# Performance work log

Measured on AMD Instinct MI355X. Metric: run time of the kernel, lower is better.

The kernel has to match this reference:

```python
import jax, jax.numpy as jnp
import numpy as np

L, H, D, V, TMAX = 6, 16, 1024, 32000, 2048
HD = D // H
EPS = 1e-5


def _ln(x, g, b):
    m = jnp.mean(x, axis=-1, keepdims=True)
    v = jnp.var(x, axis=-1, keepdims=True)
    return (x - m) * jax.lax.rsqrt(v + EPS) * g + b


def setup_inputs() -> dict:
    key = jax.random.key(0)
    ks = jax.random.split(key, 16)
    s = 0.02
    inp = {
        'idx': jax.random.randint(ks[0], (2, TMAX), 0, V),
        'targets': jax.random.randint(ks[1], (2, TMAX), 0, V),
        'tok_emb': jax.random.normal(ks[2], (V, D), jnp.float32) * s,
        'pos_emb': jax.random.normal(ks[3], (TMAX, D), jnp.float32) * s,
        'wq': jax.random.normal(ks[4], (L, D, D), jnp.float32) * s,
        'wk': jax.random.normal(ks[5], (L, D, D), jnp.float32) * s,
        'wv': jax.random.normal(ks[6], (L, D, D), jnp.float32) * s,
        'w_proj': jax.random.normal(ks[7], (L, D, D), jnp.float32) * s,
        'b_proj': jnp.zeros((L, D), jnp.float32),
        'w_fc1': jax.random.normal(ks[8], (L, D, 4 * D), jnp.float32) * s,
        'b_fc1': jnp.zeros((L, 4 * D), jnp.float32),
        'w_fc2': jax.random.normal(ks[9], (L, 4 * D, D), jnp.float32) * s,
        'b_fc2': jnp.zeros((L, D), jnp.float32),
        'ln1_g': jnp.ones((L, D), jnp.float32), 'ln1_b': jnp.zeros((L, D), jnp.float32),
        'ln2_g': jnp.ones((L, D), jnp.float32), 'ln2_b': jnp.zeros((L, D), jnp.float32),
        'lnf_g': jnp.ones((D,), jnp.float32), 'lnf_b': jnp.zeros((D,), jnp.float32),
        'w_head': jax.random.normal(ks[10], (D, V), jnp.float32) * s,
        'b_head': jnp.zeros((V,), jnp.float32),
    }
    return inp


def reference(idx, targets, tok_emb, pos_emb, wq, wk, wv, w_proj, b_proj,
              w_fc1, b_fc1, w_fc2, b_fc2, ln1_g, ln1_b, ln2_g, ln2_b,
              lnf_g, lnf_b, w_head, b_head):
    B, T = idx.shape
    x = tok_emb[idx] + pos_emb[:T]  # [B,T,D]
    causal = jnp.tril(jnp.ones((T, T), bool))
    scale = HD ** -0.5
    for l in range(L):
        h = _ln(x, ln1_g[l], ln1_b[l])
        q = (h @ wq[l]).reshape(B, T, H, HD)
        k = (h @ wk[l]).reshape(B, T, H, HD)
        v = (h @ wv[l]).reshape(B, T, H, HD)
        att = jnp.einsum('bqhd,bkhd->bhqk', q, k) * scale
        att = jnp.where(causal, att, -jnp.inf)
        att = jax.nn.softmax(att, axis=-1)  # dropout is identity in eval
        o = jnp.einsum('bhqk,bkhd->bqhd', att, v).reshape(B, T, D)
        x = x + o @ w_proj[l] + b_proj[l]
        h = _ln(x, ln2_g[l], ln2_b[l])
        x = x + jax.nn.relu(h @ w_fc1[l] + b_fc1[l]) @ w_fc2[l] + b_fc2[l]
    x = _ln(x, lnf_g, lnf_b)
    logits = x @ w_head + b_head  # [B,T,V]
    logp = jax.nn.log_softmax(logits, axis=-1)
    nll = -jnp.take_along_axis(logp, targets[..., None], axis=-1)[..., 0]
    loss = jnp.mean(nll)
    return logits, loss
```

## Files before the change

kernel.cpp:

```cpp
#include <hip/hip_runtime.h>

#define LAYERS 6
#define NH 16
#define DIM 1024
#define VOCAB 32000
#define SEQ 2048
#define NBATCH 2
#define HEADD 64
#define NROW (NBATCH*SEQ)
#define FF 4096
#define QKVS 3072
#define NCB (VOCAB/256)
#define LN_EPS 1e-5f

typedef unsigned short bfu;
typedef __attribute__((ext_vector_type(8))) short s16x8;
typedef __attribute__((ext_vector_type(4))) float f32x4;

__device__ __forceinline__ float bf2f(bfu u) { return __uint_as_float(((unsigned)u) << 16); }
__device__ __forceinline__ bfu f2bf(float x) {
  unsigned u = __float_as_uint(x);
  return (bfu)((u + 0x7fffu + ((u >> 16) & 1u)) >> 16);
}

__device__ __forceinline__ void gload16(const void* g, void* l) {
  __builtin_amdgcn_global_load_lds((const __attribute__((address_space(1))) void*)g,
                                   (__attribute__((address_space(3))) void*)l, 16, 0, 0);
}

__device__ __forceinline__ f32x4 mfma32(s16x8 a, s16x8 b, f32x4 c) {
  return __builtin_amdgcn_mfma_f32_16x16x32_bf16(a, b, c, 0, 0, 0);
}

__global__ __launch_bounds__(256) void tkernel(const float* __restrict__ in,
                                               bfu* __restrict__ out, int R, int C) {
  __shared__ bfu tile[32][33];
  int tx = threadIdx.x, ty = threadIdx.y;
  int bx = blockIdx.x * 32, by = blockIdx.y * 32;
#pragma unroll
  for (int i = 0; i < 4; ++i)
    tile[ty + i * 8][tx] = f2bf(in[(size_t)(by + ty + i * 8) * C + bx + tx]);
  __syncthreads();
#pragma unroll
  for (int i = 0; i < 4; ++i)
    out[(size_t)(bx + ty + i * 8) * R + by + tx] = tile[tx][ty + i * 8];
}

__global__ __launch_bounds__(256) void wtrans_kernel(const float* __restrict__ wq,
                                                     const float* __restrict__ wk,
                                                     const float* __restrict__ wv,
                                                     const float* __restrict__ wp,
                                                     const float* __restrict__ w1,
                                                     const float* __restrict__ w2,
                                                     bfu* __restrict__ qkvT,
                                                     bfu* __restrict__ wpT,
                                                     bfu* __restrict__ f1T,
                                                     bfu* __restrict__ f2T) {
  __shared__ bfu tile[32][33];
  int bi = blockIdx.x;
  const float* in; bfu* out; int R, C, id;
  if (bi < 4096) {
    int p = bi >> 10; id = bi & 1023;
    in = p == 0 ? wq : p == 1 ? wk : p == 2 ? wv : wp;
    out = (p == 3) ? wpT : qkvT + (size_t)p * DIM * DIM;
    R = DIM; C = DIM;
  } else if (bi < 8192) {
    id = bi - 4096; in = w1; out = f1T; R = DIM; C = FF;
  } else {
    id = bi - 8192; in = w2; out = f2T; R = FF; C = DIM;
  }
  int nbx = C >> 5;
  int bx = (id % nbx) * 32, by = (id / nbx) * 32;
  int tx = threadIdx.x, ty = threadIdx.y;
#pragma unroll
  for (int i = 0; i < 4; ++i)
    tile[ty + i * 8][tx] = f2bf(in[(size_t)(by + ty + i * 8) * C + bx + tx]);
  __syncthreads();
#pragma unroll
  for (int i = 0; i < 4; ++i)
    out[(size_t)(bx + ty + i * 8) * R + by + tx] = tile[tx][ty + i * 8];
}

__global__ __launch_bounds__(256) void vtrans_kernel(const bfu* __restrict__ qkvb,
                                                     bfu* __restrict__ vT) {
  __shared__ bfu tile[32][33];
  int bh = blockIdx.z;
  int b = bh >> 4, h = bh & 15;
  int t0 = blockIdx.x * 32, d0 = blockIdx.y * 32;
  int tx = threadIdx.x, ty = threadIdx.y;
  const bfu* in = qkvb + (size_t)b * SEQ * QKVS + 2048 + h * HEADD;
#pragma unroll
  for (int i = 0; i < 4; ++i)
    tile[ty + i * 8][tx] = in[(size_t)(t0 + ty + i * 8) * QKVS + d0 + tx];
  __syncthreads();
  bfu* out = vT + ((size_t)bh * HEADD) * SEQ;
#pragma unroll
  for (int i = 0; i < 4; ++i)
    out[(size_t)(d0 + ty + i * 8) * SEQ + t0 + tx] = tile[tx][ty + i * 8];
}

__global__ __launch_bounds__(256) void embed_kernel(const int* __restrict__ idx,
                                                    const float* __restrict__ tok,
                                                    const float* __restrict__ pos,
                                                    float* __restrict__ xf) {
  int row = blockIdx.x;
  int t = row % SEQ;
  int tokid = idx[row];
  int d0 = threadIdx.x * 4;
  float4 tv = *(const float4*)&tok[(size_t)tokid * DIM + d0];
  float4 pv = *(const float4*)&pos[(size_t)t * DIM + d0];
  float4 r;
  r.x = tv.x + pv.x; r.y = tv.y + pv.y; r.z = tv.z + pv.z; r.w = tv.w + pv.w;
  *(float4*)&xf[(size_t)row * DIM + d0] = r;
}

__global__ __launch_bounds__(256) void ln_kernel(const float* __restrict__ xf,
                                                 const float* __restrict__ gw,
                                                 const float* __restrict__ bw,
                                                 bfu* __restrict__ h) {
  const int row = blockIdx.x * 4 + (threadIdx.x >> 6);
  const int lane = threadIdx.x & 63;
  const float* xr = xf + (size_t)row * DIM;
  float4 xv[4];
  float s = 0.0f, ss = 0.0f;
#pragma unroll
  for (int j = 0; j < 4; ++j) {
    xv[j] = *(const float4*)&xr[lane * 4 + j * 256];
    s  += xv[j].x + xv[j].y + xv[j].z + xv[j].w;
    ss += xv[j].x * xv[j].x + xv[j].y * xv[j].y + xv[j].z * xv[j].z + xv[j].w * xv[j].w;
  }
#pragma unroll
  for (int o = 32; o; o >>= 1) { s += __shfl_xor(s, o); ss += __shfl_xor(ss, o); }
  float mean = s * (1.0f / DIM);
  float inv = rsqrtf(ss * (1.0f / DIM) - mean * mean + LN_EPS);
#pragma unroll
  for (int j = 0; j < 4; ++j) {
    float4 gv = *(const float4*)&gw[lane * 4 + j * 256];
    float4 bv = *(const float4*)&bw[lane * 4 + j * 256];
    ushort4 hv;
    hv.x = f2bf((xv[j].x - mean) * inv * gv.x + bv.x);
    hv.y = f2bf((xv[j].y - mean) * inv * gv.y + bv.y);
    hv.z = f2bf((xv[j].z - mean) * inv * gv.z + bv.z);
    hv.w = f2bf((xv[j].w - mean) * inv * gv.w + bv.w);
    *(ushort4*)&h[(size_t)row * DIM + lane * 4 + j * 256] = hv;
  }
}

template <int MODE>
__global__ __launch_bounds__(256) void gemm_bt(const bfu* __restrict__ A,
                                               const bfu* __restrict__ Bt,
                                               const float* __restrict__ bias,
                                               const float* resid,
                                               void* outp,
                                               int M, int N, int K) {
  __shared__ __align__(16) char sm[32768];
  const int tid = threadIdx.x;
  const int lane = tid & 63, wave = tid >> 6;
  const int c = lane & 15, g = lane >> 4;

  const int gx = gridDim.x, gy = gridDim.y;
  int orig = blockIdx.y * gx + blockIdx.x;
  int cpx = (gx * gy) >> 3;
  int swz = (orig & 7) * cpx + (orig >> 3);
  int by = swz / gx, bx = swz - by * gx;

  const int m0 = by * 128, n0 = bx * 128;
  const int wm = (wave & 1) * 64, wn = (wave >> 1) * 64;
  f32x4 acc[4][4] = {};
  const char* Ac = (const char*)A;
  const char* Bc = (const char*)Bt;
  const size_t stride = (size_t)K * 2;

  const int g1 = tid, g2 = tid + 256;
  const int r1 = g1 >> 2, j1 = g1 & 3;
  const int r2 = g2 >> 2, j2 = g2 & 3;
  const size_t a1 = (size_t)(m0 + r1) * stride + j1 * 16;
  const size_t a2 = (size_t)(m0 + r2) * stride + j2 * 16;
  const size_t b1 = (size_t)(n0 + r1) * stride + j1 * 16;
  const size_t b2 = (size_t)(n0 + r2) * stride + j2 * 16;

  auto STAGE = [&](int kt, int buf) {
    char* base = sm + buf * 16384;
    size_t ko = (size_t)kt * 64;
    gload16(Ac + a1 + ko, base + g1 * 16);
    gload16(Ac + a2 + ko, base + g2 * 16);
    gload16(Bc + b1 + ko, base + 8192 + g1 * 16);
    gload16(Bc + b2 + ko, base + 8192 + g2 * 16);
  };

  const int NT = K >> 5;
  STAGE(0, 0);
  STAGE(1, 1);
  asm volatile("s_waitcnt vmcnt(4)" ::: "memory");
  __builtin_amdgcn_s_barrier();
  __builtin_amdgcn_sched_barrier(0);

  for (int i = 0; i < NT; ++i) {
    const char* base = sm + (i & 1) * 16384;
    s16x8 af[4], bfr[4];
#pragma unroll
    for (int mi = 0; mi < 4; ++mi)
      af[mi] = *(const s16x8*)(base + (wm + mi * 16 + c) * 64 + g * 16);
#pragma unroll
    for (int ni = 0; ni < 4; ++ni)
      bfr[ni] = *(const s16x8*)(base + 8192 + (wn + ni * 16 + c) * 64 + g * 16);
    asm volatile("s_waitcnt lgkmcnt(0)" ::: "memory");
    __builtin_amdgcn_sched_barrier(0);
    __builtin_amdgcn_s_barrier();
    __builtin_amdgcn_sched_barrier(0);
    if (i + 2 < NT) STAGE(i + 2, i & 1);
    __builtin_amdgcn_s_setprio(1);
#pragma unroll
    for (int mi = 0; mi < 4; ++mi)
#pragma unroll
      for (int ni = 0; ni < 4; ++ni)
        acc[mi][ni] = mfma32(af[mi], bfr[ni], acc[mi][ni]);
    __builtin_amdgcn_s_setprio(0);
    if (i < NT - 2) {
      asm volatile("s_waitcnt vmcnt(4)" ::: "memory");
      __builtin_amdgcn_s_barrier();
      __builtin_amdgcn_sched_barrier(0);
    } else if (i == NT - 2) {
      asm volatile("s_waitcnt vmcnt(0)" ::: "memory");
      __builtin_amdgcn_s_barrier();
      __builtin_amdgcn_sched_barrier(0);
    }
  }

#pragma unroll
  for (int mi = 0; mi < 4; ++mi) {
#pragma unroll
    for (int ni = 0; ni < 4; ++ni) {
      int col = n0 + wn + ni * 16 + c;
      float bv = bias ? bias[col] : 0.0f;
#pragma unroll
      for (int jj = 0; jj < 4; ++jj) {
        int row = m0 + wm + mi * 16 + g * 4 + jj;
        float val = acc[mi][ni][jj] + bv;
        size_t oi = (size_t)row * N + col;
        if (MODE == 1) val = fmaxf(val, 0.0f);
        if (MODE == 2)      ((float*)outp)[oi] = resid[oi] + val;
        else if (MODE == 3) ((float*)outp)[oi] = val;
        else                ((bfu*)outp)[oi] = f2bf(val);
      }
    }
  }
}

template <int MODE>
__global__ __launch_bounds__(1024) void gemm1024(const bfu* __restrict__ A,
                                                 const bfu* __restrict__ Bt,
                                                 const float* __restrict__ bias,
                                                 const float* resid,
                                                 void* outp,
                                                 int M, int N, int K,
                                                 int colchunk,
                                                 float* __restrict__ pmax,
                                                 float* __restrict__ psum) {
  extern __shared__ char smem[];
  const int tid = threadIdx.x;
  const int lane = tid & 63, w = tid >> 6;
  const int c = lane & 15, g = lane >> 4;

  const int gx = gridDim.x, gy = gridDim.y;
  int orig = blockIdx.y * gx + blockIdx.x;
  int cpx = (gx * gy) >> 3;
  int swz = (orig & 7) * cpx + (orig >> 3);
  int bx, by;
  if (colchunk) { bx = swz / gy; by = swz - bx * gy; }
  else          { by = swz / gx; bx = swz - by * gx; }
  const int m0 = by * 256, n0 = bx * 256;

  const int wrow = w >> 2, wcol = w & 3;
  const size_t gstr = (size_t)K * 2;
  const char* Ag = (const char*)A + (size_t)m0 * gstr;
  const char* Bg = (const char*)Bt + (size_t)n0 * gstr;

  int srow0 = tid >> 3, scg0 = (tid & 7) ^ (srow0 & 7);
  int srow1 = (tid + 1024) >> 3, scg1 = (tid & 7) ^ (srow1 & 7);
  const size_t ga0 = (size_t)srow0 * gstr + scg0 * 16;
  const size_t ga1 = (size_t)srow1 * gstr + scg1 * 16;

  auto STAGE = [&](int kt, int buf) {
    char* base = smem + buf * 65536;
    size_t ko = (size_t)kt * 128;
    gload16(Ag + ga0 + ko, base + w * 1024);
    gload16(Ag + ga1 + ko, base + 16384 + w * 1024);
    gload16(Bg + ga0 + ko, base + 32768 + w * 1024);
    gload16(Bg + ga1 + ko, base + 49152 + w * 1024);
  };

  const int NT = K >> 6;
  f32x4 acc[4][4] = {};

  STAGE(0, 0);
  STAGE(1, 1);
  asm volatile("s_waitcnt vmcnt(4)" ::: "memory");
  __builtin_amdgcn_s_barrier();
  __builtin_amdgcn_sched_barrier(0);

  const int rsw = (c & 7) << 4;
  const int off0 = (g * 16) ^ rsw;
  const int off1 = (64 + g * 16) ^ rsw;

  for (int i = 0; i < NT; ++i) {
    const char* ldsA = smem + (i & 1) * 65536 + (wrow * 64 + c) * 128;
    const char* ldsB = smem + (i & 1) * 65536 + 32768 + (wcol * 64 + c) * 128;
    s16x8 a[4], b[4];
#pragma unroll
    for (int mi = 0; mi < 4; ++mi) a[mi] = *(const s16x8*)(ldsA + mi * 2048 + off0);
#pragma unroll
    for (int ni = 0; ni < 4; ++ni) b[ni] = *(const s16x8*)(ldsB + ni * 2048 + off0);
    __builtin_amdgcn_s_setprio(1);
#pragma unroll
    for (int mi = 0; mi < 4; ++mi)
#pragma unroll
      for (int ni = 0; ni < 4; ++ni)
        acc[mi][ni] = mfma32(a[mi], b[ni], acc[mi][ni]);
    __builtin_amdgcn_s_setprio(0);
#pragma unroll
    for (int mi = 0; mi < 4; ++mi) a[mi] = *(const s16x8*)(ldsA + mi * 2048 + off1);
#pragma unroll
    for (int ni = 0; ni < 4; ++ni) b[ni] = *(const s16x8*)(ldsB + ni * 2048 + off1);
    asm volatile("s_waitcnt lgkmcnt(0)" ::: "memory");
    __builtin_amdgcn_sched_barrier(0);
    __builtin_amdgcn_s_barrier();
    __builtin_amdgcn_sched_barrier(0);
    if (i + 2 < NT) STAGE(i + 2, i & 1);
    __builtin_amdgcn_s_setprio(1);
#pragma unroll
    for (int mi = 0; mi < 4; ++mi)
#pragma unroll
      for (int ni = 0; ni < 4; ++ni)
        acc[mi][ni] = mfma32(a[mi], b[ni], acc[mi][ni]);
    __builtin_amdgcn_s_setprio(0);
    if (i < NT - 2) {
      asm volatile("s_waitcnt vmcnt(4)" ::: "memory");
      __builtin_amdgcn_s_barrier();
      __builtin_amdgcn_sched_barrier(0);
    } else if (i == NT - 2) {
      asm volatile("s_waitcnt vmcnt(0)" ::: "memory");
      __builtin_amdgcn_s_barrier();
      __builtin_amdgcn_sched_barrier(0);
    }
  }

  if (MODE != 4) {
#pragma unroll
    for (int mi = 0; mi < 4; ++mi) {
#pragma unroll
      for (int ni = 0; ni < 4; ++ni) {
        int col = n0 + wcol * 64 + ni * 16 + c;
        float bv = bias ? bias[col] : 0.0f;
#pragma unroll
        for (int jj = 0; jj < 4; ++jj) {
          int row = m0 + wrow * 64 + mi * 16 + g * 4 + jj;
          float val = acc[mi][ni][jj] + bv;
          size_t oi = (size_t)row * N + col;
          if (MODE == 1) val = fmaxf(val, 0.0f);
          else if (MODE == 2) { ((float*)outp)[oi] = resid[oi] + val; continue; }
          if (MODE == 3) ((float*)outp)[oi] = val;
          else           ((bfu*)outp)[oi] = f2bf(val);
        }
      }
    }
  } else {
    float* sred = (float*)(smem + 131072);
    const int ncb = N >> 8;
    float bvv[4]; int colv[4];
#pragma unroll
    for (int ni = 0; ni < 4; ++ni) {
      colv[ni] = n0 + wcol * 64 + ni * 16 + c;
      bvv[ni] = bias ? bias[colv[ni]] : 0.0f;
    }
#pragma unroll
    for (int mi = 0; mi < 4; ++mi) {
#pragma unroll
      for (int jj = 0; jj < 4; ++jj) {
        int row = m0 + wrow * 64 + mi * 16 + g * 4 + jj;
        float v[4];
#pragma unroll
        for (int ni = 0; ni < 4; ++ni) {
          v[ni] = acc[mi][ni][jj] + bvv[ni];
          ((float*)outp)[(size_t)row * N + colv[ni]] = v[ni];
        }
        float mx = fmaxf(fmaxf(v[0], v[1]), fmaxf(v[2], v[3]));
#pragma unroll
        for (int off = 1; off < 16; off <<= 1) mx = fmaxf(mx, __shfl_xor(mx, off));
        float sm = __expf(v[0] - mx) + __expf(v[1] - mx) +
                   __expf(v[2] - mx) + __expf(v[3] - mx);
#pragma unroll
        for (int off = 1; off < 16; off <<= 1) sm += __shfl_xor(sm, off);
        if (c == 0) {
          int r64 = mi * 16 + g * 4 + jj;
          sred[(w * 64 + r64) * 2 + 0] = mx;
          sred[(w * 64 + r64) * 2 + 1] = sm;
        }
      }
    }
    __syncthreads();
    if (tid < 256) {
      int wr = tid >> 6, r64 = tid & 63;
      float M2 = -3.0e38f, S2 = 0.0f;
#pragma unroll
      for (int wc2 = 0; wc2 < 4; ++wc2) {
        float m_i = sred[((wr * 4 + wc2) * 64 + r64) * 2 + 0];
        float s_i = sred[((wr * 4 + wc2) * 64 + r64) * 2 + 1];
        float nm = fmaxf(M2, m_i);
        S2 = S2 * __expf(M2 - nm) + s_i * __expf(m_i - nm);
        M2 = nm;
      }
      size_t pi = (size_t)(m0 + tid) * ncb + bx;
      pmax[pi] = M2;
      psum[pi] = S2;
    }
  }
}

__global__ __launch_bounds__(512) void attn_kernel(const bfu* __restrict__ qkv,
                                                   const bfu* __restrict__ vT,
                                                   bfu* __restrict__ o) {
  __shared__ __align__(16) bfu Ks[64 * 64];
  __shared__ __align__(16) bfu Vt[64 * 64];
  __shared__ __align__(16) bfu Plds[8 * 16 * 32];
  const int tid = threadIdx.x;
  const int lane = tid & 63, w = tid >> 6;
  const int c = lane & 15, g = lane >> 4;
  const int qt = blockIdx.x, hh = blockIdx.y, b = blockIdx.z;
  const int q0 = qt * 128 + w * 16;
  const float SENT = -1e30f;
  const size_t rowb = (size_t)b * SEQ;

  const size_t qbase = (rowb + q0 + c) * QKVS + hh * HEADD + g * 8;
  s16x8 qf0 = *(const s16x8*)&qkv[qbase];
  s16x8 qf1 = *(const s16x8*)&qkv[qbase + 32];
  const bfu* Kg = qkv + 1024 + hh * HEADD;
  const bfu* vTb = vT + (size_t)(b * NH + hh) * HEADD * SEQ;
  bfu* Pw = Plds + w * 512;

  const int srow = tid >> 3;
  const int sgr = (tid & 7) ^ (srow & 7);
  const int cw = c & 7;

  f32x4 oacc[4] = {};
  float mrun = SENT, lrun = 0.0f;

  const int nkt = 2 * qt + 2;
  for (int kt = 0; kt < nkt; ++kt) {
    const int k0 = kt * 64;
    __syncthreads();
    gload16(Kg + (rowb + k0 + srow) * QKVS + sgr * 8, (char*)Ks + w * 1024);
    gload16(vTb + (size_t)srow * SEQ + k0 + sgr * 8, (char*)Vt + w * 1024);
    asm volatile("s_waitcnt vmcnt(0)" ::: "memory");
    __syncthreads();

#pragma unroll
    for (int s = 0; s < 2; ++s) {
      const int k0s = k0 + s * 32;
      if (k0s <= q0 + 15) {
        const char* Kb = (const char*)Ks + (size_t)(s * 32 + c) * 128;
        s16x8 kf00 = *(const s16x8*)(Kb + ((g ^ cw) * 16));
        s16x8 kf01 = *(const s16x8*)(Kb + (((4 + g) ^ cw) * 16));
        s16x8 kf10 = *(const s16x8*)(Kb + 16 * 128 + ((g ^ cw) * 16));
        s16x8 kf11 = *(const s16x8*)(Kb + 16 * 128 + (((4 + g) ^ cw) * 16));
        f32x4 s0 = {}, s1 = {};
        s0 = mfma32(kf00, qf0, s0); s0 = mfma32(kf01, qf1, s0);
        s1 = mfma32(kf10, qf0, s1); s1 = mfma32(kf11, qf1, s1);

        float sv[8];
#pragma unroll
        for (int jj = 0; jj < 4; ++jj) {
          int ka = k0s + g * 4 + jj, kb = ka + 16;
          sv[jj]     = (ka <= q0 + c) ? s0[jj] * 0.125f : SENT;
          sv[4 + jj] = (kb <= q0 + c) ? s1[jj] * 0.125f : SENT;
        }
        float tmax = sv[0];
#pragma unroll
        for (int i = 1; i < 8; ++i) tmax = fmaxf(tmax, sv[i]);
        tmax = fmaxf(tmax, __shfl_xor(tmax, 16));
        tmax = fmaxf(tmax, __shfl_xor(tmax, 32));

        bool defer = __all(tmax <= mrun + 8.0f) && (kt | s);
        float mref = defer ? mrun : fmaxf(mrun, tmax);
        float p[8], psm = 0.0f;
#pragma unroll
        for (int i = 0; i < 8; ++i) { p[i] = __expf(sv[i] - mref); psm += p[i]; }
        psm += __shfl_xor(psm, 16);
        psm += __shfl_xor(psm, 32);

        ushort4 w0; w0.x = f2bf(p[0]); w0.y = f2bf(p[1]); w0.z = f2bf(p[2]); w0.w = f2bf(p[3]);
        ushort4 w1; w1.x = f2bf(p[4]); w1.y = f2bf(p[5]); w1.z = f2bf(p[6]); w1.w = f2bf(p[7]);
        *(ushort4*)&Pw[c * 32 + g * 4] = w0;
        *(ushort4*)&Pw[c * 32 + 16 + g * 4] = w1;
        asm volatile("s_waitcnt lgkmcnt(0)" ::: "memory");
        __builtin_amdgcn_sched_barrier(0);

        if (defer) {
          lrun += psm;
        } else {
          float mnew = mref;
          float alpha = __expf(mrun - mnew);
          lrun = lrun * alpha + psm;
          mrun = mnew;
          float aq[4];
#pragma unroll
          for (int jj = 0; jj < 4; ++jj) aq[jj] = __shfl(alpha, g * 4 + jj);
#pragma unroll
          for (int dg = 0; dg < 4; ++dg)
#pragma unroll
            for (int jj = 0; jj < 4; ++jj) oacc[dg][jj] *= aq[jj];
        }

        ushort4 ra = *(const ushort4*)&Pw[c * 32 + g * 8];
        ushort4 rb = *(const ushort4*)&Pw[c * 32 + g * 8 + 4];
        s16x8 pa = {(short)ra.x, (short)ra.y, (short)ra.z, (short)ra.w,
                    (short)rb.x, (short)rb.y, (short)rb.z, (short)rb.w};

#pragma unroll
        for (int dg = 0; dg < 4; ++dg) {
          s16x8 vf = *(const s16x8*)((const char*)Vt + (size_t)(dg * 16 + c) * 128 +
                                     (((s * 4 + g) ^ cw) * 16));
          oacc[dg] = mfma32(pa, vf, oacc[dg]);
        }
      }
    }
  }

  float lq[4];
#pragma unroll
  for (int jj = 0; jj < 4; ++jj) lq[jj] = __shfl(lrun, g * 4 + jj);
#pragma unroll
  for (int dg = 0; dg < 4; ++dg)
#pragma unroll
    for (int jj = 0; jj < 4; ++jj) {
      size_t oi = (size_t)(rowb + q0 + g * 4 + jj) * DIM + hh * HEADD + dg * 16 + c;
      o[oi] = f2bf(oacc[dg][jj] / lq[jj]);
    }
}

__global__ __launch_bounds__(64) void nll_finish(const float* __restrict__ pmax,
                                                 const float* __restrict__ psum,
                                                 const float* __restrict__ logits,
                                                 const int* __restrict__ tgt,
                                                 float* __restrict__ nll) {
  int row = blockIdx.x, lane = threadIdx.x;
  const float* pm = pmax + (size_t)row * NCB;
  const float* ps = psum + (size_t)row * NCB;
  float m = -3.0e38f, s = 0.0f;
  if (lane < NCB) { m = pm[lane]; s = ps[lane]; }
  int i2 = lane + 64;
  if (i2 < NCB) {
    float m2 = pm[i2], s2 = ps[i2];
    float nm = fmaxf(m, m2);
    s = s * __expf(m - nm) + s2 * __expf(m2 - nm);
    m = nm;
  }
#pragma unroll
  for (int off = 32; off; off >>= 1) {
    float om = __shfl_xor(m, off), os = __shfl_xor(s, off);
    float nm = fmaxf(m, om);
    s = s * __expf(m - nm) + os * __expf(om - nm);
    m = nm;
  }
  if (lane == 0)
    nll[row] = (m + __logf(s)) - logits[(size_t)row * VOCAB + tgt[row]];
}

__global__ __launch_bounds__(256) void loss_kernel(const float* __restrict__ nll,
                                                   float* __restrict__ out) {
  float s = 0.0f;
  for (int i = threadIdx.x; i < NROW; i += 256) s += nll[i];
  for (int off = 32; off; off >>= 1) s += __shfl_xor(s, off);
  __shared__ float r[4];
  int wave = threadIdx.x >> 6;
  if ((threadIdx.x & 63) == 0) r[wave] = s;
  __syncthreads();
  if (threadIdx.x == 0) out[(size_t)NROW * VOCAB] = (r[0] + r[1] + r[2] + r[3]) * (1.0f / NROW);
}

extern "C" void kernel_launch(void* const* d_in, const int* in_sizes, int n_in,
                              void* d_out, int out_size, void* d_ws, size_t ws_size,
                              hipStream_t stream) {
  (void)in_sizes; (void)n_in; (void)out_size;
  const int* idx       = (const int*)d_in[0];
  const int* targets   = (const int*)d_in[1];
  const float* tok_emb = (const float*)d_in[2];
  const float* pos_emb = (const float*)d_in[3];
  const float* wq      = (const float*)d_in[4];
  const float* wk      = (const float*)d_in[5];
  const float* wv      = (const float*)d_in[6];
  const float* w_proj  = (const float*)d_in[7];
  const float* b_proj  = (const float*)d_in[8];
  const float* w_fc1   = (const float*)d_in[9];
  const float* b_fc1   = (const float*)d_in[10];
  const float* w_fc2   = (const float*)d_in[11];
  const float* b_fc2   = (const float*)d_in[12];
  const float* ln1_g   = (const float*)d_in[13];
  const float* ln1_b   = (const float*)d_in[14];
  const float* ln2_g   = (const float*)d_in[15];
  const float* ln2_b   = (const float*)d_in[16];
  const float* lnf_g   = (const float*)d_in[17];
  const float* lnf_b   = (const float*)d_in[18];
  const float* w_head  = (const float*)d_in[19];
  const float* b_head  = (const float*)d_in[20];

  char* ws = (char*)d_ws;
  size_t off = 0;
  auto alloc = [&](size_t bytes) {
    char* p = ws + off;
    off += (bytes + 255) & ~(size_t)255;
    return p;
  };
  float* xf   = (float*)alloc((size_t)NROW * DIM * 4);
  bfu* hbuf   = (bfu*)alloc((size_t)NROW * DIM * 2);
  bfu* qkvb   = (bfu*)alloc((size_t)NROW * QKVS * 2);
  bfu* ob     = (bfu*)alloc((size_t)NROW * DIM * 2);
  bfu* ub     = (bfu*)alloc((size_t)NROW * FF * 2);
  bfu* vT     = (bfu*)alloc((size_t)NROW * DIM * 2);
  bfu* qkvT   = (bfu*)alloc((size_t)QKVS * DIM * 2);
  bfu* wpT    = (bfu*)alloc((size_t)DIM * DIM * 2);
  bfu* f1T    = (bfu*)alloc((size_t)DIM * FF * 2);
  bfu* f2T    = (bfu*)alloc((size_t)DIM * FF * 2);
  bfu* hT     = (bfu*)alloc((size_t)DIM * VOCAB * 2);
  float* nll  = (float*)alloc((size_t)NROW * 4);
  float* pmax = (float*)alloc((size_t)NROW * NCB * 4);
  float* psum = (float*)alloc((size_t)NROW * NCB * 4);
  if (off > ws_size) return;

  const size_t LDSB = 131072;
  dim3 tb(32, 8);
  tkernel<<<dim3(VOCAB / 32, DIM / 32), tb, 0, stream>>>(w_head, hT, DIM, VOCAB);
  embed_kernel<<<NROW, 256, 0, stream>>>(idx, tok_emb, pos_emb, xf);

  float* logits = (float*)d_out;
  for (int l = 0; l < LAYERS; ++l) {
    const size_t wo = (size_t)l * DIM * DIM, fo = (size_t)l * DIM * FF;
    wtrans_kernel<<<12288, tb, 0, stream>>>(wq + wo, wk + wo, wv + wo, w_proj + wo,
                                            w_fc1 + fo, w_fc2 + fo, qkvT, wpT, f1T, f2T);
    ln_kernel<<<NROW / 4, 256, 0, stream>>>(xf, ln1_g + l * DIM, ln1_b + l * DIM, hbuf);
    gemm_bt<0><<<dim3(QKVS / 128, NROW / 128), 256, 0, stream>>>(
        hbuf, qkvT, nullptr, nullptr, qkvb, NROW, QKVS, DIM);
    vtrans_kernel<<<dim3(SEQ / 32, HEADD / 32, NBATCH * NH), tb, 0, stream>>>(qkvb, vT);
    attn_kernel<<<dim3(SEQ / 128, NH, NBATCH), 512, 0, stream>>>(qkvb, vT, ob);
    gemm_bt<2><<<dim3(DIM / 128, NROW / 128), 256, 0, stream>>>(
        ob, wpT, b_proj + l * DIM, xf, xf, NROW, DIM, DIM);
    ln_kernel<<<NROW / 4, 256, 0, stream>>>(xf, ln2_g + l * DIM, ln2_b + l * DIM, hbuf);
    gemm1024<1><<<dim3(FF / 256, NROW / 256), 1024, LDSB, stream>>>(
        hbuf, f1T, b_fc1 + l * FF, nullptr, ub, NROW, FF, DIM, 0, nullptr, nullptr);
    gemm_bt<2><<<dim3(DIM / 128, NROW / 128), 256, 0, stream>>>(
        ub, f2T, b_fc2 + l * DIM, xf, xf, NROW, DIM, FF);
  }

  ln_kernel<<<NROW / 4, 256, 0, stream>>>(xf, lnf_g, lnf_b, hbuf);
  gemm1024<4><<<dim3(VOCAB / 256, NROW / 256), 1024, LDSB + 8192, stream>>>(
      hbuf, hT, b_head, nullptr, logits, NROW, VOCAB, DIM, 1, pmax, psum);
  nll_finish<<<NROW, 64, 0, stream>>>(pmax, psum, logits, targets, nll);
  loss_kernel<<<1, 256, 0, stream>>>(nll, logits);
}
```

Baseline: 2.130 ms.

## Split-K FC2 GEMM with fused residual+LN, write V transpose from QKV GEMM

```diff
diff --git a/kernel.cpp b/kernel.cpp
--- a/kernel.cpp
+++ b/kernel.cpp
@@ -81,24 +81,6 @@
     out[(size_t)(bx + ty + i * 8) * R + by + tx] = tile[tx][ty + i * 8];
 }
 
-__global__ __launch_bounds__(256) void vtrans_kernel(const bfu* __restrict__ qkvb,
-                                                     bfu* __restrict__ vT) {
-  __shared__ bfu tile[32][33];
-  int bh = blockIdx.z;
-  int b = bh >> 4, h = bh & 15;
-  int t0 = blockIdx.x * 32, d0 = blockIdx.y * 32;
-  int tx = threadIdx.x, ty = threadIdx.y;
-  const bfu* in = qkvb + (size_t)b * SEQ * QKVS + 2048 + h * HEADD;
-#pragma unroll
-  for (int i = 0; i < 4; ++i)
-    tile[ty + i * 8][tx] = in[(size_t)(t0 + ty + i * 8) * QKVS + d0 + tx];
-  __syncthreads();
-  bfu* out = vT + ((size_t)bh * HEADD) * SEQ;
-#pragma unroll
-  for (int i = 0; i < 4; ++i)
-    out[(size_t)(d0 + ty + i * 8) * SEQ + t0 + tx] = tile[tx][ty + i * 8];
-}
-
 __global__ __launch_bounds__(256) void embed_kernel(const int* __restrict__ idx,
                                                     const float* __restrict__ tok,
                                                     const float* __restrict__ pos,
@@ -146,30 +128,80 @@
   }
 }
 
+__global__ __launch_bounds__(256) void lnfuse_kernel(float* __restrict__ xf,
+                                                     const float* __restrict__ pb,
+                                                     const float* __restrict__ bias,
+                                                     const float* __restrict__ gw,
+                                                     const float* __restrict__ bw,
+                                                     bfu* __restrict__ h) {
+  const int row = blockIdx.x * 4 + (threadIdx.x >> 6);
+  const int lane = threadIdx.x & 63;
+  float* xr = xf + (size_t)row * DIM;
+  const float* p0 = pb + (size_t)row * DIM;
+  const float* p1 = pb + (size_t)NROW * DIM + (size_t)row * DIM;
+  float4 xv[4];
+  float s = 0.0f, ss = 0.0f;
+#pragma unroll
+  for (int j = 0; j < 4; ++j) {
+    int i0 = lane * 4 + j * 256;
+    float4 a = *(const float4*)&xr[i0];
+    float4 q0 = *(const float4*)&p0[i0];
+    float4 q1 = *(const float4*)&p1[i0];
+    float4 bb = *(const float4*)&bias[i0];
+    xv[j].x = a.x + q0.x + q1.x + bb.x;
+    xv[j].y = a.y + q0.y + q1.y + bb.y;
+    xv[j].z = a.z + q0.z + q1.z + bb.z;
+    xv[j].w = a.w + q0.w + q1.w + bb.w;
+    *(float4*)&xr[i0] = xv[j];
+    s  += xv[j].x + xv[j].y + xv[j].z + xv[j].w;
+    ss += xv[j].x * xv[j].x + xv[j].y * xv[j].y + xv[j].z * xv[j].z + xv[j].w * xv[j].w;
+  }
+#pragma unroll
+  for (int o = 32; o; o >>= 1) { s += __shfl_xor(s, o); ss += __shfl_xor(ss, o); }
+  float mean = s * (1.0f / DIM);
+  float inv = rsqrtf(ss * (1.0f / DIM) - mean * mean + LN_EPS);
+#pragma unroll
+  for (int j = 0; j < 4; ++j) {
+    int i0 = lane * 4 + j * 256;
+    float4 gv = *(const float4*)&gw[i0];
+    float4 bv = *(const float4*)&bw[i0];
+    ushort4 hv;
+    hv.x = f2bf((xv[j].x - mean) * inv * gv.x + bv.x);
+    hv.y = f2bf((xv[j].y - mean) * inv * gv.y + bv.y);
+    hv.z = f2bf((xv[j].z - mean) * inv * gv.z + bv.z);
+    hv.w = f2bf((xv[j].w - mean) * inv * gv.w + bv.w);
+    *(ushort4*)&h[(size_t)row * DIM + i0] = hv;
+  }
+}
+
 template <int MODE>
 __global__ __launch_bounds__(256) void gemm_bt(const bfu* __restrict__ A,
                                                const bfu* __restrict__ Bt,
                                                const float* __restrict__ bias,
                                                const float* resid,
                                                void* outp,
-                                               int M, int N, int K) {
+                                               bfu* __restrict__ vT,
+                                               int M, int N, int K, int ldk) {
   __shared__ __align__(16) char sm[32768];
   const int tid = threadIdx.x;
   const int lane = tid & 63, wave = tid >> 6;
   const int c = lane & 15, g = lane >> 4;
 
-  const int gx = gridDim.x, gy = gridDim.y;
-  int orig = blockIdx.y * gx + blockIdx.x;
-  int cpx = (gx * gy) >> 3;
+  const int gx = gridDim.x, gy = gridDim.y, gz = gridDim.z;
+  int orig = (blockIdx.z * gy + blockIdx.y) * gx + blockIdx.x;
+  int nwg = gx * gy * gz;
+  int cpx = nwg >> 3;
   int swz = (orig & 7) * cpx + (orig >> 3);
-  int by = swz / gx, bx = swz - by * gx;
+  int bz = swz / (gx * gy);
+  int rem = swz - bz * (gx * gy);
+  int by = rem / gx, bx = rem - by * gx;
 
   const int m0 = by * 128, n0 = bx * 128;
   const int wm = (wave & 1) * 64, wn = (wave >> 1) * 64;
   f32x4 acc[4][4] = {};
-  const char* Ac = (const char*)A;
-  const char* Bc = (const char*)Bt;
-  const size_t stride = (size_t)K * 2;
+  const char* Ac = (const char*)(A + (size_t)bz * K);
+  const char* Bc = (const char*)(Bt + (size_t)bz * K);
+  const size_t stride = (size_t)ldk * 2;
 
   const int g1 = tid, g2 = tid + 256;
   const int r1 = g1 >> 2, j1 = g1 & 3;
@@ -232,7 +264,7 @@
 #pragma unroll
     for (int ni = 0; ni < 4; ++ni) {
       int col = n0 + wn + ni * 16 + c;
-      float bv = bias ? bias[col] : 0.0f;
+      float bv = (MODE != 6 && bias) ? bias[col] : 0.0f;
 #pragma unroll
       for (int jj = 0; jj < 4; ++jj) {
         int row = m0 + wm + mi * 16 + g * 4 + jj;
@@ -240,8 +272,15 @@
         size_t oi = (size_t)row * N + col;
         if (MODE == 1) val = fmaxf(val, 0.0f);
         if (MODE == 2)      ((float*)outp)[oi] = resid[oi] + val;
-        else if (MODE == 3) ((float*)outp)[oi] = val;
-        else                ((bfu*)outp)[oi] = f2bf(val);
+        else if (MODE == 6) ((float*)outp)[(size_t)bz * M * N + oi] = val;
+        else {
+          ((bfu*)outp)[oi] = f2bf(val);
+          if (MODE == 5 && col >= 2048) {
+            int d = col - 2048;
+            int b2 = row >> 11, t = row & 2047;
+            vT[((size_t)((b2 << 4) + (d >> 6)) * HEADD + (d & 63)) * SEQ + t] = f2bf(val);
+          }
+        }
       }
     }
   }
@@ -617,6 +656,7 @@
   bfu* ob     = (bfu*)alloc((size_t)NROW * DIM * 2);
   bfu* ub     = (bfu*)alloc((size_t)NROW * FF * 2);
   bfu* vT     = (bfu*)alloc((size_t)NROW * DIM * 2);
+  float* pbuf = (float*)alloc((size_t)2 * NROW * DIM * 4);
   bfu* qkvT   = (bfu*)alloc((size_t)QKVS * DIM * 2);
   bfu* wpT    = (bfu*)alloc((size_t)DIM * DIM * 2);
   bfu* f1T    = (bfu*)alloc((size_t)DIM * FF * 2);
@@ -637,21 +677,24 @@
     const size_t wo = (size_t)l * DIM * DIM, fo = (size_t)l * DIM * FF;
     wtrans_kernel<<<12288, tb, 0, stream>>>(wq + wo, wk + wo, wv + wo, w_proj + wo,
                                             w_fc1 + fo, w_fc2 + fo, qkvT, wpT, f1T, f2T);
-    ln_kernel<<<NROW / 4, 256, 0, stream>>>(xf, ln1_g + l * DIM, ln1_b + l * DIM, hbuf);
-    gemm_bt<0><<<dim3(QKVS / 128, NROW / 128), 256, 0, stream>>>(
-        hbuf, qkvT, nullptr, nullptr, qkvb, NROW, QKVS, DIM);
-    vtrans_kernel<<<dim3(SEQ / 32, HEADD / 32, NBATCH * NH), tb, 0, stream>>>(qkvb, vT);
+    if (l == 0)
+      ln_kernel<<<NROW / 4, 256, 0, stream>>>(xf, ln1_g, ln1_b, hbuf);
+    else
+      lnfuse_kernel<<<NROW / 4, 256, 0, stream>>>(xf, pbuf, b_fc2 + (l - 1) * DIM,
+                                                  ln1_g + l * DIM, ln1_b + l * DIM, hbuf);
+    gemm_bt<5><<<dim3(QKVS / 128, NROW / 128), 256, 0, stream>>>(
+        hbuf, qkvT, nullptr, nullptr, qkvb, vT, NROW, QKVS, DIM, DIM);
     attn_kernel<<<dim3(SEQ / 128, NH, NBATCH), 512, 0, stream>>>(qkvb, vT, ob);
     gemm_bt<2><<<dim3(DIM / 128, NROW / 128), 256, 0, stream>>>(
-        ob, wpT, b_proj + l * DIM, xf, xf, NROW, DIM, DIM);
+        ob, wpT, b_proj + l * DIM, xf, xf, nullptr, NROW, DIM, DIM, DIM);
     ln_kernel<<<NROW / 4, 256, 0, stream>>>(xf, ln2_g + l * DIM, ln2_b + l * DIM, hbuf);
     gemm1024<1><<<dim3(FF / 256, NROW / 256), 1024, LDSB, stream>>>(
         hbuf, f1T, b_fc1 + l * FF, nullptr, ub, NROW, FF, DIM, 0, nullptr, nullptr);
-    gemm_bt<2><<<dim3(DIM / 128, NROW / 128), 256, 0, stream>>>(
-        ub, f2T, b_fc2 + l * DIM, xf, xf, NROW, DIM, FF);
-  }
-
-  ln_kernel<<<NROW / 4, 256, 0, stream>>>(xf, lnf_g, lnf_b, hbuf);
+    gemm_bt<6><<<dim3(DIM / 128, NROW / 128, 2), 256, 0, stream>>>(
+        ub, f2T, nullptr, nullptr, pbuf, nullptr, NROW, DIM, FF / 2, FF);
+  }
+
+  lnfuse_kernel<<<NROW / 4, 256, 0, stream>>>(xf, pbuf, b_fc2 + 5 * DIM, lnf_g, lnf_b, hbuf);
   gemm1024<4><<<dim3(VOCAB / 256, NROW / 256), 1024, LDSB + 8192, stream>>>(
       hbuf, hT, b_head, nullptr, logits, NROW, VOCAB, DIM, 1, pmax, psum);
   nll_finish<<<NROW, 64, 0, stream>>>(pmax, psum, logits, targets, nll);
```

New measurement: 2.018 ms. 1.06x faster.
